# Performance work log

Hardware: AMD Instinct MI355X
Metric: run time of the kernel (lower is better)

## Reference

```python
import jax, jax.numpy as jnp
import numpy as np

EPS = 1e-5


def _bn(h, gamma, beta):
    # BatchNorm1d, training mode: biased batch statistics over nodes
    mu = jnp.mean(h, axis=0)
    var = jnp.mean(jnp.square(h - mu), axis=0)
    return (h - mu) * jax.lax.rsqrt(var + EPS) * gamma + beta


def setup_inputs() -> dict:
    key = jax.random.key(0)
    ks = jax.random.split(key, 12)
    N, E, D, H = 50000, 800000, 128, 256
    x = jax.random.normal(ks[0], (N, D), dtype=jnp.float32)
    edge_index = jax.random.randint(ks[1], (2, E), 0, N, dtype=jnp.int64)
    train_node_id = jax.random.randint(ks[2], (10000,), 0, N, dtype=jnp.int64)
    def lin(k, fan_in, fan_out):
        bound = 1.0 / np.sqrt(fan_in)
        return jax.random.uniform(k, (fan_in, fan_out), jnp.float32, -bound, bound)
    return {
        "x": x, "edge_index": edge_index, "train_node_id": train_node_id,
        "W1": lin(ks[3], D, H), "b1": jnp.zeros((H,), jnp.float32),
        "W2": lin(ks[4], H, H), "b2": jnp.zeros((H,), jnp.float32),
        "W3": lin(ks[5], H, H), "b3": jnp.zeros((H,), jnp.float32),
        "g1": jnp.ones((H,), jnp.float32), "be1": jnp.zeros((H,), jnp.float32),
        "g2": jnp.ones((H,), jnp.float32), "be2": jnp.zeros((H,), jnp.float32),
        "g3": jnp.ones((H,), jnp.float32), "be3": jnp.zeros((H,), jnp.float32),
        "Wl": lin(ks[6], H, H), "bl": jnp.zeros((H,), jnp.float32),
        "Wf": lin(ks[7], H, 1), "bf": jnp.zeros((1,), jnp.float32),
    }


def reference(x, edge_index, train_node_id, W1, b1, W2, b2, W3, b3,
              g1, be1, g2, be2, g3, be3, Wl, bl, Wf, bf):
    N = x.shape[0]
    loops = jnp.arange(N, dtype=edge_index.dtype)
    row = jnp.concatenate([edge_index[0], loops])  # destinations
    col = jnp.concatenate([edge_index[1], loops])  # sources
    deg = jax.ops.segment_sum(jnp.ones_like(row, dtype=x.dtype), row, num_segments=N)
    d_isqrt = jax.lax.rsqrt(deg)  # deg >= 1 due to self loops
    norm = (d_isqrt[row] * d_isqrt[col])[:, None]  # [E+N, 1]

    def gcn(h, W, b):
        hW = h @ W
        agg = jax.ops.segment_sum(hW[col] * norm, row, num_segments=N)
        return agg + b

    h = jax.nn.relu(_bn(gcn(x, W1, b1), g1, be1))
    h = jax.nn.relu(_bn(gcn(h, W2, b2), g2, be2))
    h = jax.nn.relu(_bn(gcn(h, W3, b3), g3, be3))
    h = jax.nn.relu(h @ Wl + bl)
    h = h[train_node_id]
    return jnp.squeeze(h @ Wf + bf, -1)
```

## Files before the change

### kernel.cpp

```cpp
#include <hip/hip_runtime.h>

typedef unsigned short u16;
typedef __attribute__((ext_vector_type(8))) short short8;
typedef __attribute__((ext_vector_type(4))) float f32x4;

#define GPB 25

#define DEVFN static __device__ __forceinline__

DEVFN u16 f2b(float f) {
    union { float f; unsigned v; } x; x.f = f;
    unsigned r = x.v + 0x7fffu + ((x.v >> 16) & 1u);
    return (u16)(r >> 16);
}

DEVFN int detect64(const int* __restrict__ p) {
    int orv = 0;
#pragma unroll
    for (int i = 1; i < 64; i += 2) orv |= p[i];
    return (orv == 0) ? 1 : 0;
}

DEVFN unsigned get_xcc() {
    unsigned x;
    asm volatile("s_getreg_b32 %0, hwreg(HW_REG_XCC_ID)" : "=s"(x));
    return x & 7u;
}

DEVFN void accum_row8(short8 v, float* acc) {
    const unsigned* u = (const unsigned*)&v;
#pragma unroll
    for (int k = 0; k < 4; k++) {
        union { float f; unsigned w; } lo, hi;
        lo.w = u[k] << 16;
        hi.w = u[k] & 0xffff0000u;
        acc[2 * k] += lo.f;
        acc[2 * k + 1] += hi.f;
    }
}

__global__ void k_init(const float* __restrict__ W1, const float* __restrict__ W2,
                       const float* __restrict__ W3, const float* __restrict__ Wl,
                       u16* __restrict__ T1, u16* __restrict__ T2,
                       u16* __restrict__ T3, u16* __restrict__ Tl,
                       int* __restrict__ z9,
                       float* __restrict__ stat, float* __restrict__ out, int N, int M) {
    int t = blockIdx.x * 256 + threadIdx.x;
    int Z = (N * 9) / 4;
    if (t < 229376) {
        const float* W; u16* T; int K; int idx;
        if (t < 32768)        { W = W1; T = T1; K = 128; idx = t; }
        else if (t < 98304)   { W = W2; T = T2; K = 256; idx = t - 32768; }
        else if (t < 163840)  { W = W3; T = T3; K = 256; idx = t - 98304; }
        else                  { W = Wl; T = Tl; K = 256; idx = t - 163840; }
        int k = idx >> 8, n = idx & 255;
        T[(size_t)n * K + k] = f2b(W[(size_t)k * 256 + n]);
    } else if (t < 229376 + Z) {
        ((int4*)z9)[t - 229376] = (int4){0, 0, 0, 0};
    } else if (t < 229376 + Z + 384) {
        ((float4*)stat)[t - 229376 - Z] = (float4){0.f, 0.f, 0.f, 0.f};
    } else if (t < 229376 + Z + 384 + (M + 3) / 4) {
        int i = (t - 229376 - Z - 384) * 4;
        if (i + 3 < M) *(float4*)(out + i) = (float4){0.f, 0.f, 0.f, 0.f};
        else for (int k = i; k < M; k++) out[k] = 0.f;
    }
}

__global__ void k_fillb(const int* __restrict__ ei, unsigned* __restrict__ cnt8,
                        int* __restrict__ ovfc, u16* __restrict__ slots8,
                        u16* __restrict__ ovf, int E) {
    int fl = detect64(ei);
    unsigned xcc = get_xcc();
    int t = blockIdx.x * 256 + threadIdx.x;
    int e0 = t * 2;
    if (e0 >= E) return;
    int r0, r1, c0, c1;
    bool two = (e0 + 1 < E);
    if (fl) {
        const int4* p4 = (const int4*)ei;
        int4 d = p4[t];
        int4 s = p4[(E >> 1) + t];
        r0 = d.x; r1 = d.z; c0 = s.x; c1 = s.z;
    } else {
        const int2* p2 = (const int2*)ei;
        int2 d = p2[t];
        int2 s = p2[(E >> 1) + t];
        r0 = d.x; r1 = d.y; c0 = s.x; c1 = s.y;
    }
    {
        unsigned p = __hip_atomic_fetch_add(&cnt8[(size_t)r0 * 8 + xcc], 1u,
                                            __ATOMIC_RELAXED, __HIP_MEMORY_SCOPE_WORKGROUP);
        if (p < 8) slots8[(size_t)r0 * 64 + xcc * 8 + p] = (u16)c0;
        else { int q = atomicAdd(&ovfc[r0], 1); if (q < 64) ovf[(size_t)r0 * 64 + q] = (u16)c0; }
    }
    if (two) {
        unsigned p = __hip_atomic_fetch_add(&cnt8[(size_t)r1 * 8 + xcc], 1u,
                                            __ATOMIC_RELAXED, __HIP_MEMORY_SCOPE_WORKGROUP);
        if (p < 8) slots8[(size_t)r1 * 64 + xcc * 8 + p] = (u16)c1;
        else { int q = atomicAdd(&ovfc[r1], 1); if (q < 64) ovf[(size_t)r1 * 64 + q] = (u16)c1; }
    }
}

__global__ __launch_bounds__(256) void k_prep(
        const unsigned* __restrict__ cnt8, int* __restrict__ ovfc,
        const u16* __restrict__ slots8, int* __restrict__ cnt,
        u16* __restrict__ slots, u16* __restrict__ ovf,
        const float* __restrict__ x, float* __restrict__ disq,
        u16* __restrict__ xb, int N, int CB) {
    int b = blockIdx.x;
    if (b < CB) {
        int lane = threadIdx.x & 63;
        int wv = threadIdx.x >> 6;
        int j = lane >> 2;
        int p = lane & 3;
        int d = b * 64 + wv * 16 + j;
        bool valid = d < N;
        int dd = valid ? d : (N - 1);
        int2 c2 = *(const int2*)(cnt8 + (size_t)dd * 8 + p * 2);
        int nA = min(c2.x, 8), nB = min(c2.y, 8);
        int v = nA + nB;
        int w = c2.x + c2.y;
        int j4 = lane & ~3;
        int v0 = __shfl(v, j4 + 0, 64);
        int v1 = __shfl(v, j4 + 1, 64);
        int v2 = __shfl(v, j4 + 2, 64);
        int base = (p > 0 ? v0 : 0) + (p > 1 ? v1 : 0) + (p > 2 ? v2 : 0);
        int wsum = w;
        wsum += __shfl_xor(wsum, 1, 64);
        wsum += __shfl_xor(wsum, 2, 64);
        const u16* s8 = slots8 + (size_t)dd * 64 + p * 16;
        u16* sd = slots + (size_t)dd * 32;
        if (valid) {
            for (int i = 0; i < nA; i++) {
                int pos = base + i; u16 val = s8[i];
                if (pos < 32) sd[pos] = val;
                else { int q = atomicAdd(&ovfc[dd], 1); if (q < 64) ovf[(size_t)dd * 64 + q] = val; }
            }
            for (int i = 0; i < nB; i++) {
                int pos = base + nA + i; u16 val = s8[8 + i];
                if (pos < 32) sd[pos] = val;
                else { int q = atomicAdd(&ovfc[dd], 1); if (q < 64) ovf[(size_t)dd * 64 + q] = val; }
            }
            if (p == 3) {
                int selfpos = base + nA + nB;
                if (selfpos < 32) sd[selfpos] = (u16)dd;
                else { int q = atomicAdd(&ovfc[dd], 1); if (q < 64) ovf[(size_t)dd * 64 + q] = (u16)dd; }
                int dc = min(selfpos + 1, 32);
                int tot = min(wsum + 1, dc + 64);
                cnt[dd] = dc | (tot << 8);
            }
        }
    } else {
        int tt = (b - CB) * 256 + threadIdx.x;
        if (tt >= N * 32) return;
        int row = tt >> 5;
        int f0 = (tt & 31) * 4;
        const unsigned* c8 = cnt8 + (size_t)row * 8;
        unsigned s = 0;
#pragma unroll
        for (int k = 0; k < 8; k++) s += c8[k];
        float dq = rsqrtf((float)(s + 1));
        if ((tt & 31) == 0) disq[row] = dq;
        float4 vx = *(const float4*)(x + (size_t)row * 128 + f0);
        ushort4 o;
        o.x = f2b(vx.x * dq); o.y = f2b(vx.y * dq); o.z = f2b(vx.z * dq); o.w = f2b(vx.w * dq);
        *(ushort4*)(xb + (size_t)(f0 >> 5) * N * 32 + (size_t)row * 32 + (f0 & 31)) = o;
    }
}

template<int PBITS>
__global__ __launch_bounds__(256) void k_gatherP(
        const u16* __restrict__ src, const int* __restrict__ cnt,
        const u16* __restrict__ slots, const u16* __restrict__ ovf,
        const float* __restrict__ disq, u16* __restrict__ dst, int N) {
    const int NP = 1 << PBITS;
    const size_t N32 = (size_t)N * 32;
    int plane = blockIdx.x & (NP - 1);
    int lane = threadIdx.x & 63;
    int wv = threadIdx.x >> 6;
    int j = lane >> 2;
    int piece = lane & 3;
    int dbase = (blockIdx.x >> PBITS) * 64 + wv * 16;
    int d = dbase + j;
    bool live = d < N;
    int packed = live ? cnt[d] : 0;
    int dc = packed & 0xff;
    int tot = packed >> 8;
    float di = live ? disq[d] : 0.f;

    short8 sb = *(const short8*)(slots + (size_t)dbase * 32 + lane * 8);
    const unsigned* sbw = (const unsigned*)&sb;

    const u16* sbase = src + (size_t)plane * N32 + piece * 8;
    const u16* ov = ovf + (size_t)d * 64;

    float acc[8] = {0.f, 0.f, 0.f, 0.f, 0.f, 0.f, 0.f, 0.f};

    int m = dc;
    m = max(m, __shfl_xor(m, 4, 64));
    m = max(m, __shfl_xor(m, 8, 64));
    m = max(m, __shfl_xor(m, 16, 64));
    m = max(m, __shfl_xor(m, 32, 64));

    for (int rb = 0; rb < 4; rb++) {
        int r0 = rb * 8;
        if (r0 >= m) break;
        int srcl = j * 4 + rb;
        int cs[8];
#pragma unroll
        for (int rw = 0; rw < 4; rw++) {
            unsigned w = (unsigned)__shfl((int)sbw[rw], srcl, 64);
#pragma unroll
            for (int hh = 0; hh < 2; hh++) {
                int r = r0 + rw * 2 + hh;
                u16 s = hh ? (u16)(w >> 16) : (u16)(w & 0xffffu);
                cs[rw * 2 + hh] = (r < dc) ? (int)s : -1;
            }
        }
        short8 vs[8];
#pragma unroll
        for (int k = 0; k < 8; k++)
            if (cs[k] >= 0) vs[k] = *(const short8*)(sbase + (size_t)cs[k] * 32);
#pragma unroll
        for (int k = 0; k < 8; k++)
            if (cs[k] >= 0) accum_row8(vs[k], acc);
    }

    int nov = tot - dc;
    int novm = nov;
    novm = max(novm, __shfl_xor(novm, 4, 64));
    novm = max(novm, __shfl_xor(novm, 8, 64));
    novm = max(novm, __shfl_xor(novm, 16, 64));
    novm = max(novm, __shfl_xor(novm, 32, 64));
    for (int r = 0; r < novm; r++) {
        if (r < nov) {
            int c = (int)ov[r];
            short8 v = *(const short8*)(sbase + (size_t)c * 32);
            accum_row8(v, acc);
        }
    }

    if (live) {
        short8 o;
        u16* op = (u16*)&o;
#pragma unroll
        for (int k = 0; k < 8; k++) op[k] = f2b(acc[k] * di);
        __builtin_nontemporal_store(o,
            (short8*)(dst + (size_t)plane * N32 + (size_t)d * 32 + piece * 8));
    }
}

template<int KS>
__global__ __launch_bounds__(256, 2) void k_gemm_rb(
        const u16* __restrict__ A, const u16* __restrict__ Wt,
        float* __restrict__ Cf, int PS, int Gtot,
        float* __restrict__ stat, const float* __restrict__ bias,
        const float* __restrict__ Wfp, const float* __restrict__ bfp,
        float* __restrict__ outp) {
    constexpr int K = KS * 32;
    __shared__ float sbuf[4][2][64];
    int wv = threadIdx.x >> 6;
    int lane = threadIdx.x & 63;
    int quad = lane >> 4;
    int mr = lane & 15;
    int colbase = blockIdx.y * 64;
    int g0 = blockIdx.x * GPB;

    short8 Bf[4][KS];
#pragma unroll
    for (int j = 0; j < 4; j++)
#pragma unroll
        for (int s = 0; s < KS; s++)
            Bf[j][s] = *(const short8*)(Wt + (size_t)(colbase + j * 16 + mr) * K + s * 32 + quad * 8);

    float4 bv4[4], wf4[4];
    if (Wfp) {
#pragma unroll
        for (int j = 0; j < 4; j++) {
            bv4[j] = *(const float4*)(bias + colbase + j * 16 + quad * 4);
            wf4[j] = *(const float4*)(Wfp + colbase + j * 16 + quad * 4);
        }
    }

    f32x4 sreg[4], s2reg[4];
#pragma unroll
    for (int j = 0; j < 4; j++) {
        sreg[j] = (f32x4){0.f, 0.f, 0.f, 0.f};
        s2reg[j] = (f32x4){0.f, 0.f, 0.f, 0.f};
    }

    for (int g = wv; g < GPB; g += 4) {
        int gg = g0 + g;
        if (gg >= Gtot) continue;
        int row = gg * 16 + mr;
        const u16* Ap = A + (size_t)row * 32 + quad * 8;

        short8 Af[KS];
#pragma unroll
        for (int s = 0; s < KS; s++) Af[s] = *(const short8*)(Ap + (size_t)s * PS);

        f32x4 acc[4];
#pragma unroll
        for (int j = 0; j < 4; j++) acc[j] = (f32x4){0.f, 0.f, 0.f, 0.f};
#pragma unroll
        for (int s = 0; s < KS; s++)
#pragma unroll
            for (int j = 0; j < 4; j++)
                acc[j] = __builtin_amdgcn_mfma_f32_16x16x32_bf16(Bf[j][s], Af[s], acc[j], 0, 0, 0);

        if (Wfp) {
            float pr = 0.f;
#pragma unroll
            for (int j = 0; j < 4; j++) {
                const float* bj = (const float*)&bv4[j];
                const float* wj = (const float*)&wf4[j];
#pragma unroll
                for (int r = 0; r < 4; r++) {
                    float v = fmaxf(acc[j][r] + bj[r], 0.f);
                    pr += v * wj[r];
                }
            }
            pr += __shfl_xor(pr, 16, 64);
            pr += __shfl_xor(pr, 32, 64);
            if (quad == 0) {
                float v = pr;
                if (blockIdx.y == 0) v += bfp[0];
                atomicAdd(&outp[row], v);
            }
            continue;
        }

        float* cp = Cf + (size_t)row * 256 + colbase + quad * 4;
#pragma unroll
        for (int j = 0; j < 4; j++) {
            *(f32x4*)(cp + j * 16) = acc[j];
            sreg[j] += acc[j];
            s2reg[j] += acc[j] * acc[j];
        }
    }

    if (stat) {
#pragma unroll
        for (int j = 0; j < 4; j++) {
#pragma unroll
            for (int r = 0; r < 4; r++) {
                float a = sreg[j][r], b = s2reg[j][r];
                a += __shfl_xor(a, 1, 64); b += __shfl_xor(b, 1, 64);
                a += __shfl_xor(a, 2, 64); b += __shfl_xor(b, 2, 64);
                a += __shfl_xor(a, 4, 64); b += __shfl_xor(b, 4, 64);
                a += __shfl_xor(a, 8, 64); b += __shfl_xor(b, 8, 64);
                if (mr == 0) {
                    sbuf[wv][0][j * 16 + quad * 4 + r] = a;
                    sbuf[wv][1][j * 16 + quad * 4 + r] = b;
                }
            }
        }
        __syncthreads();
        int t = threadIdx.x;
        if (t < 128) {
            int which = t >> 6, c = t & 63;
            float v = sbuf[0][which][c] + sbuf[1][which][c] +
                      sbuf[2][which][c] + sbuf[3][which][c];
            atomicAdd(&stat[which * 256 + colbase + c], v);
        }
    }
}


__global__ void k_bnapply(const float* __restrict__ t, const float* __restrict__ stat,
                          const float* __restrict__ gamma, const float* __restrict__ beta,
                          u16* __restrict__ h, int N, float invN,
                          const float* __restrict__ scale) {
    size_t tt = (size_t)blockIdx.x * 256 + threadIdx.x;
    size_t base = tt * 4;
    if (base >= (size_t)N * 256) return;
    int f0 = (int)(base & 255);
    int row = (int)(base >> 8);
    float sc2 = scale ? scale[row] : 1.0f;
    float4 v = *(const float4*)(t + base);
    float r[4] = {v.x, v.y, v.z, v.w};
    ushort4 o;
    u16* op = (u16*)&o;
#pragma unroll
    for (int j = 0; j < 4; j++) {
        int f = f0 + j;
        float mean = stat[f] * invN;
        float var = stat[256 + f] * invN - mean * mean;
        float rstd = rsqrtf(var + 1e-5f);
        float sc = rstd * gamma[f];
        float sh = beta[f] - mean * sc;
        op[j] = f2b(fmaxf(r[j] * sc + sh, 0.0f) * sc2);
    }
    *(ushort4*)(h + (size_t)(f0 >> 5) * N * 32 + (size_t)row * 32 + (f0 & 31)) = o;
}

__global__ void k_bnapply_idx(const float* __restrict__ t, const float* __restrict__ stat,
                              const float* __restrict__ gamma, const float* __restrict__ beta,
                              const int* __restrict__ idx, u16* __restrict__ zin,
                              int M, float invN) {
    int fl = detect64(idx);
    size_t tt = (size_t)blockIdx.x * 256 + threadIdx.x;
    size_t base = tt * 4;
    if (base >= (size_t)M * 256) return;
    int f0 = (int)(base & 255);
    int row = (int)(base >> 8);
    int node = idx[(size_t)row << fl];
    float4 v = *(const float4*)(t + (size_t)node * 256 + f0);
    float r[4] = {v.x, v.y, v.z, v.w};
    ushort4 o;
    u16* op = (u16*)&o;
#pragma unroll
    for (int j = 0; j < 4; j++) {
        int f = f0 + j;
        float mean = stat[f] * invN;
        float var = stat[256 + f] * invN - mean * mean;
        float rstd = rsqrtf(var + 1e-5f);
        float sc = rstd * gamma[f];
        float sh = beta[f] - mean * sc;
        op[j] = f2b(fmaxf(r[j] * sc + sh, 0.0f));
    }
    *(ushort4*)(zin + (size_t)(f0 >> 5) * M * 32 + (size_t)row * 32 + (f0 & 31)) = o;
}


extern "C" void kernel_launch(void* const* d_in, const int* in_sizes, int n_in,
                              void* d_out, int out_size, void* d_ws, size_t ws_size,
                              hipStream_t stream) {
    const int D = 128, H = 256;
    const int N = in_sizes[0] / D;
    const int E = in_sizes[1] / 2;
    const int M = in_sizes[2];

    const float* x = (const float*)d_in[0];
    const int* ei = (const int*)d_in[1];
    const int* tnid = (const int*)d_in[2];
    const float* W1 = (const float*)d_in[3];
    const float* W2 = (const float*)d_in[5];
    const float* W3 = (const float*)d_in[7];
    const float* g1 = (const float*)d_in[9];
    const float* be1 = (const float*)d_in[10];
    const float* g2 = (const float*)d_in[11];
    const float* be2 = (const float*)d_in[12];
    const float* g3 = (const float*)d_in[13];
    const float* be3 = (const float*)d_in[14];
    const float* Wl = (const float*)d_in[15];
    const float* bl = (const float*)d_in[16];
    const float* Wf = (const float*)d_in[17];
    const float* bfp = (const float*)d_in[18];
    float* out = (float*)d_out;

    char* w = (char*)d_ws;
    size_t off = 0;
    auto carve = [&](size_t bytes) -> void* {
        void* p = w + off;
        off = (off + bytes + 255) & ~(size_t)255;
        return p;
    };

    float* stat = (float*)carve(3 * 512 * 4);
    float* disq = (float*)carve((size_t)N * 4);
    int* cnt = (int*)carve((size_t)N * 4);
    u16* slots = (u16*)carve((size_t)N * 32 * 2);
    u16* ovf = (u16*)carve((size_t)N * 64 * 2);
    u16* Wt1 = (u16*)carve((size_t)H * D * 2);
    u16* Wt2 = (u16*)carve((size_t)H * H * 2);
    u16* Wt3 = (u16*)carve((size_t)H * H * 2);
    u16* Wtl = (u16*)carve((size_t)H * H * 2);
    u16* xb = (u16*)carve((size_t)N * D * 2);
    u16* aggx = (u16*)carve((size_t)N * D * 2);
    u16* aggh = (u16*)carve((size_t)N * H * 2);
    float* tb = (float*)carve((size_t)N * H * 4);
    u16* hb = (u16*)carve((size_t)N * H * 2);
    u16* zin = (u16*)carve((size_t)M * H * 2);

    unsigned* cnt8 = (unsigned*)hb;
    int* ovfc = (int*)(hb + (size_t)N * 8 * 2);
    u16* slots8 = (u16*)tb;

    const float invN = 1.0f / (float)N;

    const int Gn = N / 16;
    const int Gm = M / 16;
    dim3 gemm_grid((Gn + GPB - 1) / GPB, 4);
    dim3 gemm_grid_m((Gm + GPB - 1) / GPB, 4);
    const int PSn = N * 32;
    const int PSm = M * 32;
    const int chunks = (N + 63) / 64;
    const int PB = (int)(((size_t)N * H / 4 + 255) / 256);
    const int PBm = (int)(((size_t)M * H / 4 + 255) / 256);
    const int CB = chunks;
    const int XB = (N * 32 + 255) / 256;
    const int initT = 229376 + (N * 9) / 4 + 384 + (M + 3) / 4;

    k_init<<<(initT + 255) / 256, 256, 0, stream>>>(
        W1, W2, W3, Wl, Wt1, Wt2, Wt3, Wtl, (int*)cnt8, stat, out, N, M);
    k_fillb<<<(E / 2 + 255) / 256, 256, 0, stream>>>(ei, cnt8, ovfc, slots8, ovf, E);
    k_prep<<<CB + XB, 256, 0, stream>>>(cnt8, ovfc, slots8, cnt, slots, ovf, x, disq, xb, N, CB);

    k_gatherP<2><<<4 * chunks, 256, 0, stream>>>(xb, cnt, slots, ovf, disq, aggx, N);
    k_gemm_rb<4><<<gemm_grid, 256, 0, stream>>>(aggx, Wt1, tb, PSn, Gn, stat, nullptr, nullptr, nullptr, nullptr);
    k_bnapply<<<PB, 256, 0, stream>>>(tb, stat, g1, be1, hb, N, invN, disq);
    k_gatherP<3><<<8 * chunks, 256, 0, stream>>>(hb, cnt, slots, ovf, disq, aggh, N);
    k_gemm_rb<8><<<gemm_grid, 256, 0, stream>>>(aggh, Wt2, tb, PSn, Gn, stat + 512, nullptr, nullptr, nullptr, nullptr);
    k_bnapply<<<PB, 256, 0, stream>>>(tb, stat + 512, g2, be2, hb, N, invN, disq);
    k_gatherP<3><<<8 * chunks, 256, 0, stream>>>(hb, cnt, slots, ovf, disq, aggh, N);
    k_gemm_rb<8><<<gemm_grid, 256, 0, stream>>>(aggh, Wt3, tb, PSn, Gn, stat + 1024, nullptr, nullptr, nullptr, nullptr);
    k_bnapply_idx<<<PBm, 256, 0, stream>>>(tb, stat + 1024, g3, be3, tnid, zin, M, invN);

    k_gemm_rb<8><<<gemm_grid_m, 256, 0, stream>>>(zin, Wtl, nullptr, PSm, Gm, nullptr, bl, Wf, bfp, out);
}
```

Before: 416.0 us.

## Replace global-atomic edge binning with LDS-atomic range/segment binning

Replaces the per-XCC global atomic edge fill with a kernel that splits nodes into 8 ranges and edges into 64 segments. Each block counts its range's edges in shared memory and writes slots into per-(node,segment) cells of capacity 4. The prep kernel then compacts these cells into the 32-slot CSR-like layout, so overflow offsets no longer need atomics. This targets global atomic contention. In exchange every block reads its whole edge segment once per range (8x edge reads), and the intermediate cell buffer is larger.

```diff
diff --git a/kernel.cpp b/kernel.cpp
--- a/kernel.cpp
+++ b/kernel.cpp
@@ -1,10 +1,14 @@
 #include <hip/hip_runtime.h>
 
 typedef unsigned short u16;
+typedef unsigned char u8;
 typedef __attribute__((ext_vector_type(8))) short short8;
 typedef __attribute__((ext_vector_type(4))) float f32x4;
 
 #define GPB 25
+#define RANGES 8
+#define SEGS 64
+#define BCAP 4
 
 #define DEVFN static __device__ __forceinline__
 
@@ -19,12 +23,6 @@
 #pragma unroll
     for (int i = 1; i < 64; i += 2) orv |= p[i];
     return (orv == 0) ? 1 : 0;
-}
-
-DEVFN unsigned get_xcc() {
-    unsigned x;
-    asm volatile("s_getreg_b32 %0, hwreg(HW_REG_XCC_ID)" : "=s"(x));
-    return x & 7u;
 }
 
 DEVFN void accum_row8(short8 v, float* acc) {
@@ -43,10 +41,12 @@
                        const float* __restrict__ W3, const float* __restrict__ Wl,
                        u16* __restrict__ T1, u16* __restrict__ T2,
                        u16* __restrict__ T3, u16* __restrict__ Tl,
-                       int* __restrict__ z9,
+                       int* __restrict__ cz,
+                       int* __restrict__ oz,
                        float* __restrict__ stat, float* __restrict__ out, int N, int M) {
     int t = blockIdx.x * 256 + threadIdx.x;
-    int Z = (N * 9) / 4;
+    int A = N * 4;
+    int B = N / 4;
     if (t < 229376) {
         const float* W; u16* T; int K; int idx;
         if (t < 32768)        { W = W1; T = T1; K = 128; idx = t; }
@@ -55,55 +55,60 @@
         else                  { W = Wl; T = Tl; K = 256; idx = t - 163840; }
         int k = idx >> 8, n = idx & 255;
         T[(size_t)n * K + k] = f2b(W[(size_t)k * 256 + n]);
-    } else if (t < 229376 + Z) {
-        ((int4*)z9)[t - 229376] = (int4){0, 0, 0, 0};
-    } else if (t < 229376 + Z + 384) {
-        ((float4*)stat)[t - 229376 - Z] = (float4){0.f, 0.f, 0.f, 0.f};
-    } else if (t < 229376 + Z + 384 + (M + 3) / 4) {
-        int i = (t - 229376 - Z - 384) * 4;
+    } else if (t < 229376 + A) {
+        ((int4*)cz)[t - 229376] = (int4){0, 0, 0, 0};
+    } else if (t < 229376 + A + B) {
+        ((int4*)oz)[t - 229376 - A] = (int4){0, 0, 0, 0};
+    } else if (t < 229376 + A + B + 384) {
+        ((float4*)stat)[t - 229376 - A - B] = (float4){0.f, 0.f, 0.f, 0.f};
+    } else if (t < 229376 + A + B + 384 + (M + 3) / 4) {
+        int i = (t - 229376 - A - B - 384) * 4;
         if (i + 3 < M) *(float4*)(out + i) = (float4){0.f, 0.f, 0.f, 0.f};
         else for (int k = i; k < M; k++) out[k] = 0.f;
     }
 }
 
-__global__ void k_fillb(const int* __restrict__ ei, unsigned* __restrict__ cnt8,
-                        int* __restrict__ ovfc, u16* __restrict__ slots8,
-                        u16* __restrict__ ovf, int E) {
+__global__ __launch_bounds__(256) void k_bin(
+        const int* __restrict__ ei, u16* __restrict__ slot_seg,
+        u8* __restrict__ cnt_seg, int* __restrict__ ovfc,
+        u16* __restrict__ ovf, int E, int N, int rng) {
+    __shared__ unsigned lc[6336];
     int fl = detect64(ei);
-    unsigned xcc = get_xcc();
-    int t = blockIdx.x * 256 + threadIdx.x;
-    int e0 = t * 2;
-    if (e0 >= E) return;
-    int r0, r1, c0, c1;
-    bool two = (e0 + 1 < E);
-    if (fl) {
-        const int4* p4 = (const int4*)ei;
-        int4 d = p4[t];
-        int4 s = p4[(E >> 1) + t];
-        r0 = d.x; r1 = d.z; c0 = s.x; c1 = s.z;
-    } else {
-        const int2* p2 = (const int2*)ei;
-        int2 d = p2[t];
-        int2 s = p2[(E >> 1) + t];
-        r0 = d.x; r1 = d.y; c0 = s.x; c1 = s.y;
-    }
-    {
-        unsigned p = __hip_atomic_fetch_add(&cnt8[(size_t)r0 * 8 + xcc], 1u,
-                                            __ATOMIC_RELAXED, __HIP_MEMORY_SCOPE_WORKGROUP);
-        if (p < 8) slots8[(size_t)r0 * 64 + xcc * 8 + p] = (u16)c0;
-        else { int q = atomicAdd(&ovfc[r0], 1); if (q < 64) ovf[(size_t)r0 * 64 + q] = (u16)c0; }
-    }
-    if (two) {
-        unsigned p = __hip_atomic_fetch_add(&cnt8[(size_t)r1 * 8 + xcc], 1u,
-                                            __ATOMIC_RELAXED, __HIP_MEMORY_SCOPE_WORKGROUP);
-        if (p < 8) slots8[(size_t)r1 * 64 + xcc * 8 + p] = (u16)c1;
-        else { int q = atomicAdd(&ovfc[r1], 1); if (q < 64) ovf[(size_t)r1 * 64 + q] = (u16)c1; }
+    int rg = blockIdx.x & (RANGES - 1);
+    int sg = blockIdx.x >> 3;
+    int rbase = rg * rng;
+    for (int k = threadIdx.x; k < rng; k += 256) lc[k] = 0;
+    __syncthreads();
+    int seglen = (E + SEGS - 1) / SEGS;
+    int s0 = sg * seglen;
+    int s1 = min(s0 + seglen, E);
+    for (int idx = s0 + threadIdx.x; idx < s1; idx += 256) {
+        int r, c;
+        if (fl) {
+            r = ((const int2*)ei)[idx].x;
+            c = ((const int2*)ei)[E + idx].x;
+        } else {
+            r = ei[idx];
+            c = ei[E + idx];
+        }
+        int lr = r - rbase;
+        if ((unsigned)lr < (unsigned)rng) {
+            unsigned p = atomicAdd(&lc[lr], 1u);
+            if (p < BCAP) slot_seg[((size_t)r * SEGS + sg) * BCAP + p] = (u16)c;
+            else { int q = atomicAdd(&ovfc[r], 1); if (q < 64) ovf[(size_t)r * 64 + q] = (u16)c; }
+        }
+    }
+    __syncthreads();
+    for (int k = threadIdx.x; k < rng; k += 256) {
+        int node = rbase + k;
+        unsigned c = lc[k];
+        if (node < N && c) cnt_seg[(size_t)node * SEGS + sg] = (u8)min(c, 255u);
     }
 }
 
 __global__ __launch_bounds__(256) void k_prep(
-        const unsigned* __restrict__ cnt8, int* __restrict__ ovfc,
-        const u16* __restrict__ slots8, int* __restrict__ cnt,
+        const u8* __restrict__ cnt_seg, const int* __restrict__ ovfc,
+        const u16* __restrict__ slot_seg, int* __restrict__ cnt,
         u16* __restrict__ slots, u16* __restrict__ ovf,
         const float* __restrict__ x, float* __restrict__ disq,
         u16* __restrict__ xb, int N, int CB) {
@@ -116,37 +121,49 @@
         int d = b * 64 + wv * 16 + j;
         bool valid = d < N;
         int dd = valid ? d : (N - 1);
-        int2 c2 = *(const int2*)(cnt8 + (size_t)dd * 8 + p * 2);
-        int nA = min(c2.x, 8), nB = min(c2.y, 8);
-        int v = nA + nB;
-        int w = c2.x + c2.y;
+        int4 ci = ((const int4*)(cnt_seg + (size_t)dd * SEGS))[p];
+        unsigned cw[4] = {(unsigned)ci.x, (unsigned)ci.y, (unsigned)ci.z, (unsigned)ci.w};
+        int ns = 0;
+#pragma unroll
+        for (int q = 0; q < 16; q++)
+            ns += min((int)((cw[q >> 2] >> ((q & 3) * 8)) & 255u), BCAP);
         int j4 = lane & ~3;
-        int v0 = __shfl(v, j4 + 0, 64);
-        int v1 = __shfl(v, j4 + 1, 64);
-        int v2 = __shfl(v, j4 + 2, 64);
-        int base = (p > 0 ? v0 : 0) + (p > 1 ? v1 : 0) + (p > 2 ? v2 : 0);
-        int wsum = w;
-        wsum += __shfl_xor(wsum, 1, 64);
-        wsum += __shfl_xor(wsum, 2, 64);
-        const u16* s8 = slots8 + (size_t)dd * 64 + p * 16;
-        u16* sd = slots + (size_t)dd * 32;
+        int n0 = __shfl(ns, j4 + 0, 64);
+        int n1 = __shfl(ns, j4 + 1, 64);
+        int n2 = __shfl(ns, j4 + 2, 64);
+        int base = (p > 0 ? n0 : 0) + (p > 1 ? n1 : 0) + (p > 2 ? n2 : 0);
+        int avail = __shfl(base + ns, j4 + 3, 64);
+        int spilled = valid ? min(ovfc[dd], 64) : 0;
         if (valid) {
-            for (int i = 0; i < nA; i++) {
-                int pos = base + i; u16 val = s8[i];
-                if (pos < 32) sd[pos] = val;
-                else { int q = atomicAdd(&ovfc[dd], 1); if (q < 64) ovf[(size_t)dd * 64 + q] = val; }
-            }
-            for (int i = 0; i < nB; i++) {
-                int pos = base + nA + i; u16 val = s8[8 + i];
-                if (pos < 32) sd[pos] = val;
-                else { int q = atomicAdd(&ovfc[dd], 1); if (q < 64) ovf[(size_t)dd * 64 + q] = val; }
+            short8 cells[8];
+            const short8* cp8 = (const short8*)(slot_seg + (size_t)dd * (SEGS * BCAP) + p * 64);
+#pragma unroll
+            for (int q = 0; q < 8; q++) cells[q] = cp8[q];
+            u16* sd = slots + (size_t)dd * 32;
+            u16* ovp = ovf + (size_t)dd * 64;
+            int pos = base;
+#pragma unroll
+            for (int q = 0; q < 8; q++) {
+                const u16* ce = (const u16*)&cells[q];
+#pragma unroll
+                for (int h = 0; h < 2; h++) {
+                    int sidx = q * 2 + h;
+                    int c = (int)((cw[sidx >> 2] >> ((sidx & 3) * 8)) & 255u);
+                    int n = min(c, BCAP);
+                    for (int i = 0; i < n; i++) {
+                        u16 val = ce[h * 4 + i];
+                        if (pos < 32) sd[pos] = val;
+                        else { int qq = spilled + pos - 32; if (qq < 64) ovp[qq] = val; }
+                        pos++;
+                    }
+                }
             }
             if (p == 3) {
-                int selfpos = base + nA + nB;
+                int selfpos = avail;
                 if (selfpos < 32) sd[selfpos] = (u16)dd;
-                else { int q = atomicAdd(&ovfc[dd], 1); if (q < 64) ovf[(size_t)dd * 64 + q] = (u16)dd; }
-                int dc = min(selfpos + 1, 32);
-                int tot = min(wsum + 1, dc + 64);
+                else { int qq = spilled + selfpos - 32; if (qq < 64) ovp[qq] = (u16)dd; }
+                int dc = min(avail + 1, 32);
+                int tot = min(avail + 1 + spilled, dc + 64);
                 cnt[dd] = dc | (tot << 8);
             }
         }
@@ -154,13 +171,17 @@
         int tt = (b - CB) * 256 + threadIdx.x;
         if (tt >= N * 32) return;
         int row = tt >> 5;
-        int f0 = (tt & 31) * 4;
-        const unsigned* c8 = cnt8 + (size_t)row * 8;
-        unsigned s = 0;
-#pragma unroll
-        for (int k = 0; k < 8; k++) s += c8[k];
+        int l = tt & 31;
+        unsigned v = *(const u16*)(cnt_seg + (size_t)row * SEGS + l * 2);
+        int s = (int)(v & 255u) + (int)(v >> 8);
+        s += __shfl_xor(s, 1, 64);
+        s += __shfl_xor(s, 2, 64);
+        s += __shfl_xor(s, 4, 64);
+        s += __shfl_xor(s, 8, 64);
+        s += __shfl_xor(s, 16, 64);
         float dq = rsqrtf((float)(s + 1));
-        if ((tt & 31) == 0) disq[row] = dq;
+        if (l == 0) disq[row] = dq;
+        int f0 = l * 4;
         float4 vx = *(const float4*)(x + (size_t)row * 128 + f0);
         ushort4 o;
         o.x = f2b(vx.x * dq); o.y = f2b(vx.y * dq); o.z = f2b(vx.z * dq); o.w = f2b(vx.w * dq);
@@ -473,9 +494,9 @@
     u16* hb = (u16*)carve((size_t)N * H * 2);
     u16* zin = (u16*)carve((size_t)M * H * 2);
 
-    unsigned* cnt8 = (unsigned*)hb;
-    int* ovfc = (int*)(hb + (size_t)N * 8 * 2);
-    u16* slots8 = (u16*)tb;
+    u16* slot_seg = (u16*)tb;
+    u8* cnt_seg = (u8*)tb + (size_t)N * SEGS * BCAP * 2;
+    int* ovfc = (int*)hb;
 
     const float invN = 1.0f / (float)N;
 
@@ -490,12 +511,13 @@
     const int PBm = (int)(((size_t)M * H / 4 + 255) / 256);
     const int CB = chunks;
     const int XB = (N * 32 + 255) / 256;
-    const int initT = 229376 + (N * 9) / 4 + 384 + (M + 3) / 4;
+    const int rng = (N + RANGES - 1) / RANGES;
+    const int initT = 229376 + N * 4 + N / 4 + 384 + (M + 3) / 4;
 
     k_init<<<(initT + 255) / 256, 256, 0, stream>>>(
-        W1, W2, W3, Wl, Wt1, Wt2, Wt3, Wtl, (int*)cnt8, stat, out, N, M);
-    k_fillb<<<(E / 2 + 255) / 256, 256, 0, stream>>>(ei, cnt8, ovfc, slots8, ovf, E);
-    k_prep<<<CB + XB, 256, 0, stream>>>(cnt8, ovfc, slots8, cnt, slots, ovf, x, disq, xb, N, CB);
+        W1, W2, W3, Wl, Wt1, Wt2, Wt3, Wtl, (int*)cnt_seg, ovfc, stat, out, N, M);
+    k_bin<<<RANGES * SEGS, 256, 0, stream>>>(ei, slot_seg, cnt_seg, ovfc, ovf, E, N, rng);
+    k_prep<<<CB + XB, 256, 0, stream>>>(cnt_seg, ovfc, slot_seg, cnt, slots, ovf, x, disq, xb, N, CB);
 
     k_gatherP<2><<<4 * chunks, 256, 0, stream>>>(xb, cnt, slots, ovf, disq, aggx, N);
     k_gemm_rb<4><<<gemm_grid, 256, 0, stream>>>(aggx, Wt1, tb, PSn, Gn, stat, nullptr, nullptr, nullptr, nullptr);
```

Measured after the change: 460.9 us. +10.8%, slower.

## Use per-XCC plane layout for edge bucketing and scan-based compaction

Applied to the files above, without the earlier changes.

Edge bucket counters and slot cells move from a node-major layout with eight XCC sub-bins per node to one plane per XCC (xcc*N + node). Atomics from one XCC then land in a contiguous region instead of sharing cache lines with other XCCs' counters. The prep kernel now compacts with an 8-lane shuffle prefix scan and one vector load of each slot cell. Overflow positions come from the scan offsets plus the spill count from fill, which replaces the per-edge atomicAdd fallback. Degree sums use lane shuffles, and scratch is carved from tb, whose size must cover the new planes.

```diff
diff --git a/kernel.cpp b/kernel.cpp
--- a/kernel.cpp
+++ b/kernel.cpp
@@ -1,10 +1,12 @@
 #include <hip/hip_runtime.h>
 
 typedef unsigned short u16;
+typedef unsigned char u8;
 typedef __attribute__((ext_vector_type(8))) short short8;
 typedef __attribute__((ext_vector_type(4))) float f32x4;
 
 #define GPB 25
+#define SCAP 8
 
 #define DEVFN static __device__ __forceinline__
 
@@ -66,11 +68,12 @@
     }
 }
 
-__global__ void k_fillb(const int* __restrict__ ei, unsigned* __restrict__ cnt8,
-                        int* __restrict__ ovfc, u16* __restrict__ slots8,
-                        u16* __restrict__ ovf, int E) {
+__global__ void k_fill(const int* __restrict__ ei, unsigned* __restrict__ cntp,
+                       int* __restrict__ ovfc, u16* __restrict__ slotp,
+                       u16* __restrict__ ovf, int E, int N) {
     int fl = detect64(ei);
     unsigned xcc = get_xcc();
+    size_t pbase = (size_t)xcc * N;
     int t = blockIdx.x * 256 + threadIdx.x;
     int e0 = t * 2;
     if (e0 >= E) return;
@@ -88,22 +91,22 @@
         r0 = d.x; r1 = d.y; c0 = s.x; c1 = s.y;
     }
     {
-        unsigned p = __hip_atomic_fetch_add(&cnt8[(size_t)r0 * 8 + xcc], 1u,
+        unsigned p = __hip_atomic_fetch_add(&cntp[pbase + r0], 1u,
                                             __ATOMIC_RELAXED, __HIP_MEMORY_SCOPE_WORKGROUP);
-        if (p < 8) slots8[(size_t)r0 * 64 + xcc * 8 + p] = (u16)c0;
+        if (p < SCAP) slotp[(pbase + r0) * SCAP + p] = (u16)c0;
         else { int q = atomicAdd(&ovfc[r0], 1); if (q < 64) ovf[(size_t)r0 * 64 + q] = (u16)c0; }
     }
     if (two) {
-        unsigned p = __hip_atomic_fetch_add(&cnt8[(size_t)r1 * 8 + xcc], 1u,
+        unsigned p = __hip_atomic_fetch_add(&cntp[pbase + r1], 1u,
                                             __ATOMIC_RELAXED, __HIP_MEMORY_SCOPE_WORKGROUP);
-        if (p < 8) slots8[(size_t)r1 * 64 + xcc * 8 + p] = (u16)c1;
+        if (p < SCAP) slotp[(pbase + r1) * SCAP + p] = (u16)c1;
         else { int q = atomicAdd(&ovfc[r1], 1); if (q < 64) ovf[(size_t)r1 * 64 + q] = (u16)c1; }
     }
 }
 
 __global__ __launch_bounds__(256) void k_prep(
-        const unsigned* __restrict__ cnt8, int* __restrict__ ovfc,
-        const u16* __restrict__ slots8, int* __restrict__ cnt,
+        const unsigned* __restrict__ cntp, const int* __restrict__ ovfc,
+        const u16* __restrict__ slotp, int* __restrict__ cnt,
         u16* __restrict__ slots, u16* __restrict__ ovf,
         const float* __restrict__ x, float* __restrict__ disq,
         u16* __restrict__ xb, int N, int CB) {
@@ -111,56 +114,57 @@
     if (b < CB) {
         int lane = threadIdx.x & 63;
         int wv = threadIdx.x >> 6;
-        int j = lane >> 2;
-        int p = lane & 3;
-        int d = b * 64 + wv * 16 + j;
-        bool valid = d < N;
-        int dd = valid ? d : (N - 1);
-        int2 c2 = *(const int2*)(cnt8 + (size_t)dd * 8 + p * 2);
-        int nA = min(c2.x, 8), nB = min(c2.y, 8);
-        int v = nA + nB;
-        int w = c2.x + c2.y;
-        int j4 = lane & ~3;
-        int v0 = __shfl(v, j4 + 0, 64);
-        int v1 = __shfl(v, j4 + 1, 64);
-        int v2 = __shfl(v, j4 + 2, 64);
-        int base = (p > 0 ? v0 : 0) + (p > 1 ? v1 : 0) + (p > 2 ? v2 : 0);
-        int wsum = w;
-        wsum += __shfl_xor(wsum, 1, 64);
-        wsum += __shfl_xor(wsum, 2, 64);
-        const u16* s8 = slots8 + (size_t)dd * 64 + p * 16;
-        u16* sd = slots + (size_t)dd * 32;
-        if (valid) {
-            for (int i = 0; i < nA; i++) {
-                int pos = base + i; u16 val = s8[i];
+        int ns = lane >> 3;
+        int sh = lane & 7;
+        int d = b * 32 + wv * 8 + ns;
+        if (d >= N) return;
+        size_t po = (size_t)sh * N + d;
+        int craw = (int)cntp[po];
+        int cl = min(craw, SCAP);
+        short8 cell = *(const short8*)(slotp + po * SCAP);
+        const u16* ep = (const u16*)&cell;
+        int s = cl;
+#pragma unroll
+        for (int i = 1; i < 8; i <<= 1) {
+            int v = __shfl_up(s, i, 64);
+            if (sh >= i) s += v;
+        }
+        int P = s - cl;
+        int avail = __shfl(s, lane | 7, 64);
+        int spilled = min(ovfc[d], 64);
+        u16* sd = slots + (size_t)d * 32;
+        u16* ovp = ovf + (size_t)d * 64;
+#pragma unroll
+        for (int i = 0; i < SCAP; i++) {
+            if (i < cl) {
+                int pos = P + i;
+                u16 val = ep[i];
                 if (pos < 32) sd[pos] = val;
-                else { int q = atomicAdd(&ovfc[dd], 1); if (q < 64) ovf[(size_t)dd * 64 + q] = val; }
+                else { int qq = spilled + pos - 32; if (qq < 64) ovp[qq] = val; }
             }
-            for (int i = 0; i < nB; i++) {
-                int pos = base + nA + i; u16 val = s8[8 + i];
-                if (pos < 32) sd[pos] = val;
-                else { int q = atomicAdd(&ovfc[dd], 1); if (q < 64) ovf[(size_t)dd * 64 + q] = val; }
-            }
-            if (p == 3) {
-                int selfpos = base + nA + nB;
-                if (selfpos < 32) sd[selfpos] = (u16)dd;
-                else { int q = atomicAdd(&ovfc[dd], 1); if (q < 64) ovf[(size_t)dd * 64 + q] = (u16)dd; }
-                int dc = min(selfpos + 1, 32);
-                int tot = min(wsum + 1, dc + 64);
-                cnt[dd] = dc | (tot << 8);
-            }
+        }
+        if (sh == 7) {
+            int selfpos = avail;
+            if (selfpos < 32) sd[selfpos] = (u16)d;
+            else { int qq = spilled + selfpos - 32; if (qq < 64) ovp[qq] = (u16)d; }
+            int dc = min(avail + 1, 32);
+            int tot = min(avail + 1 + spilled, dc + 64);
+            cnt[d] = dc | (tot << 8);
         }
     } else {
         int tt = (b - CB) * 256 + threadIdx.x;
         if (tt >= N * 32) return;
         int row = tt >> 5;
-        int f0 = (tt & 31) * 4;
-        const unsigned* c8 = cnt8 + (size_t)row * 8;
-        unsigned s = 0;
-#pragma unroll
-        for (int k = 0; k < 8; k++) s += c8[k];
+        int l = tt & 31;
+        int s = (l < 8) ? (int)cntp[(size_t)l * N + row] : 0;
+        s += __shfl_xor(s, 1, 64);
+        s += __shfl_xor(s, 2, 64);
+        s += __shfl_xor(s, 4, 64);
+        s += __shfl_xor(s, 8, 64);
+        s += __shfl_xor(s, 16, 64);
         float dq = rsqrtf((float)(s + 1));
-        if ((tt & 31) == 0) disq[row] = dq;
+        if (l == 0) disq[row] = dq;
+        int f0 = l * 4;
         float4 vx = *(const float4*)(x + (size_t)row * 128 + f0);
         ushort4 o;
         o.x = f2b(vx.x * dq); o.y = f2b(vx.y * dq); o.z = f2b(vx.z * dq); o.w = f2b(vx.w * dq);
@@ -473,9 +477,9 @@
     u16* hb = (u16*)carve((size_t)N * H * 2);
     u16* zin = (u16*)carve((size_t)M * H * 2);
 
-    unsigned* cnt8 = (unsigned*)hb;
-    int* ovfc = (int*)(hb + (size_t)N * 8 * 2);
-    u16* slots8 = (u16*)tb;
+    unsigned* cntp = (unsigned*)tb;
+    int* ovfc = (int*)(cntp + (size_t)8 * N);
+    u16* slotp = (u16*)(ovfc + N);
 
     const float invN = 1.0f / (float)N;
 
@@ -488,14 +492,14 @@
     const int chunks = (N + 63) / 64;
     const int PB = (int)(((size_t)N * H / 4 + 255) / 256);
     const int PBm = (int)(((size_t)M * H / 4 + 255) / 256);
-    const int CB = chunks;
+    const int CB = (N + 31) / 32;
     const int XB = (N * 32 + 255) / 256;
     const int initT = 229376 + (N * 9) / 4 + 384 + (M + 3) / 4;
 
     k_init<<<(initT + 255) / 256, 256, 0, stream>>>(
-        W1, W2, W3, Wl, Wt1, Wt2, Wt3, Wtl, (int*)cnt8, stat, out, N, M);
-    k_fillb<<<(E / 2 + 255) / 256, 256, 0, stream>>>(ei, cnt8, ovfc, slots8, ovf, E);
-    k_prep<<<CB + XB, 256, 0, stream>>>(cnt8, ovfc, slots8, cnt, slots, ovf, x, disq, xb, N, CB);
+        W1, W2, W3, Wl, Wt1, Wt2, Wt3, Wtl, (int*)cntp, stat, out, N, M);
+    k_fill<<<(E / 2 + 255) / 256, 256, 0, stream>>>(ei, cntp, ovfc, slotp, ovf, E, N);
+    k_prep<<<CB + XB, 256, 0, stream>>>(cntp, ovfc, slotp, cnt, slots, ovf, x, disq, xb, N, CB);
 
     k_gatherP<2><<<4 * chunks, 256, 0, stream>>>(xb, cnt, slots, ovf, disq, aggx, N);
     k_gemm_rb<4><<<gemm_grid, 256, 0, stream>>>(aggx, Wt1, tb, PSn, Gn, stat, nullptr, nullptr, nullptr, nullptr);
```

Result: faster. 401.4 us (-3.5%).
